# Performance work log

Hardware: AMD Instinct MI355X
Metric: run time of the kernel (lower is better)

Reference implementation:

```python
import jax, jax.numpy as jnp
import numpy as np

B, S, P = 64, 1024, 1024
D_IN, D, OUT = 50, 300, 1024
LN_EPS = 1e-6  # custom LayerNorm in repo-style code (a_2/b_2, eps=1e-6)


def setup_inputs() -> dict:
    key = jax.random.key(0)
    ks = jax.random.split(key, 16)
    std = 1e-4  # matches torch .normal_(mean=0, std=0.0001)
    return {
        "x": jax.random.normal(ks[0], (B, S, D_IN), jnp.float32),
        "matrix_embed": jax.random.normal(ks[1], (D_IN, D), jnp.float32),
        "past": jax.random.normal(ks[2], (B, P, D_IN), jnp.float32),
        "w_pt": jax.random.normal(ks[3], (D_IN, D), jnp.float32) * std,
        "b_pt": jax.random.normal(ks[4], (1, D), jnp.float32) * std,
        "w_pg": jax.random.normal(ks[5], (D_IN, D), jnp.float32) * std,
        "b_pg": jax.random.normal(ks[6], (1, D), jnp.float32) * std,
        "w_ps": jax.random.normal(ks[7], (D_IN, D), jnp.float32) * std,
        "b_ps": jax.random.normal(ks[8], (1, D), jnp.float32) * std,
        "w_ex": jax.random.normal(ks[9], (D_IN, D), jnp.float32) * std,
        "b_ex": jax.random.normal(ks[10], (1, D), jnp.float32) * std,
        "ln_g": jnp.ones((D,), jnp.float32),
        "ln_b": jnp.zeros((D,), jnp.float32),
        "W1": jax.random.normal(ks[11], (D, D), jnp.float32) * 0.05,
        "b1": jnp.zeros((D,), jnp.float32),
        "W2": jax.random.normal(ks[12], (D, OUT), jnp.float32) * 0.05,
        "b2": jnp.zeros((OUT,), jnp.float32),
    }


def _layernorm(h, g, b):
    mu = jnp.mean(h, axis=-1, keepdims=True)
    var = jnp.mean(jnp.square(h - mu), axis=-1, keepdims=True)
    return g * (h - mu) / jnp.sqrt(var + LN_EPS) + b


def reference(x, matrix_embed, past, w_pt, b_pt, w_pg, b_pg, w_ps, b_ps,
              w_ex, b_ex, ln_g, ln_b, W1, b1, W2, b2):
    # token: [B,S,300]
    token = _layernorm(x @ matrix_embed, ln_g, ln_b)
    past_token = jnp.tanh(x @ w_pt + b_pt)          # [B,S,300]
    past_vector = jnp.tanh(past @ w_pg + b_pg)      # [B,P,300]
    past_gate = jax.nn.sigmoid(jnp.einsum('bsd,bpd->bsp', past_token, past_vector))
    past_state = jnp.tanh(past @ w_ps + b_ps)       # [B,P,300]
    pre_state = past_gate @ past_state              # [B,S,300]
    expose_vector = jnp.tanh(x @ w_ex + b_ex)       # [B,S,300]
    expose_gate = jax.nn.sigmoid(jnp.einsum('bsd,btd->bst', expose_vector, pre_state))
    filter_token = token + expose_gate @ pre_state  # [B,S,300]
    # output MLP (dropout is identity in eval mode)
    h = jax.nn.relu(filter_token @ W1 + b1)
    return h @ W2 + b2
```

## Files before the change

kernel.cpp:

```cpp
#include <hip/hip_runtime.h>
#include <hip/hip_bf16.h>
#include <math.h>

typedef __attribute__((ext_vector_type(8))) short bf16x8;
typedef __attribute__((ext_vector_type(4))) float f32x4;

__device__ inline float bf2f(short u) {
  union { float f; unsigned int i; } v;
  v.i = ((unsigned int)(unsigned short)u) << 16;
  return v.f;
}
__device__ inline short f2bf(float f) {
  union { float f; unsigned int i; } v; v.f = f;
  unsigned int r = v.i + 0x7fff + ((v.i >> 16) & 1);
  return (short)(r >> 16);
}

__global__ void pad_rows(const float* __restrict__ src, short* __restrict__ dst,
                         int C, int Cp, int total) {
  int i = blockIdx.x * 256 + threadIdx.x;
  if (i >= total) return;
  int r = i / Cp, c = i - r * Cp;
  dst[i] = f2bf(c < C ? src[(size_t)r * C + c] : 0.f);
}

__global__ void pad_T(const float* __restrict__ src, short* __restrict__ dst,
                      int K, int N, int Kp, int total) {
  int i = blockIdx.x * 256 + threadIdx.x;
  if (i >= total) return;
  int n = i / Kp, k = i - n * Kp;
  dst[i] = f2bf((k < K && n < N) ? src[(size_t)k * N + n] : 0.f);
}

__global__ __launch_bounds__(256) void transpose_pd(const short* __restrict__ in,
                                                    short* __restrict__ out) {
  __shared__ unsigned int T[64][32];
  const int b = blockIdx.z, p0 = blockIdx.x * 64, d0 = blockIdx.y * 64;
  const short* ib = in + (size_t)b * 1024 * 320;
  short* ob = out + (size_t)b * 320 * 1024;
  for (int i = threadIdx.x; i < 512; i += 256) {
    int p = i >> 3, g = i & 7;
    uint4 v = *(const uint4*)&ib[(size_t)(p0 + p) * 320 + d0 + g * 8];
    int s = p & 31;
    T[p][(4 * g + 0) ^ s] = v.x;
    T[p][(4 * g + 1) ^ s] = v.y;
    T[p][(4 * g + 2) ^ s] = v.z;
    T[p][(4 * g + 3) ^ s] = v.w;
  }
  __syncthreads();
  for (int i = threadIdx.x; i < 512; i += 256) {
    int d = i >> 3, g = i & 7;
    int w0 = d >> 1;
    __align__(16) unsigned short tmp[8];
#pragma unroll
    for (int j = 0; j < 8; ++j) {
      int p = g * 8 + j;
      unsigned int val = T[p][w0 ^ (p & 31)];
      tmp[j] = (d & 1) ? (unsigned short)(val >> 16) : (unsigned short)(val & 0xffff);
    }
    *(uint4*)&ob[(size_t)(d0 + d) * 1024 + p0 + g * 8] = *(const uint4*)tmp;
  }
}

template<int NT, int MODE>
__global__ __launch_bounds__(512) void gemm_ep(
    const short* __restrict__ A, const short* __restrict__ Bt, int K,
    const float* __restrict__ bias, int biasN,
    void* __restrict__ outp, int outStride)
{
  __shared__ __align__(16) short Bst[NT][40];
  const int tid = threadIdx.x;
  const int wave = tid >> 6, lane = tid & 63;
  const int m = lane & 15, quad = lane >> 4;
  const int row0 = blockIdx.x * 128 + wave * 16;
  const int n0 = blockIdx.y * NT;

  f32x4 zero = {0.f, 0.f, 0.f, 0.f};
  f32x4 acc[NT / 16];
#pragma unroll
  for (int i = 0; i < NT / 16; ++i) acc[i] = zero;

  const short* arow = A + (size_t)(row0 + m) * K;

  for (int k0 = 0; k0 < K; k0 += 32) {
    __syncthreads();
    for (int idx = tid; idx < NT * 4; idx += 512) {
      int n = idx >> 2, kc = (idx & 3) << 3;
      *(uint4*)&Bst[n][kc] = *(const uint4*)&Bt[(size_t)(n0 + n) * K + k0 + kc];
    }
    __syncthreads();
    bf16x8 af = *(const bf16x8*)(arow + k0 + quad * 8);
#pragma unroll
    for (int nt = 0; nt < NT / 16; ++nt) {
      bf16x8 bf = *(const bf16x8*)&Bst[nt * 16 + m][quad * 8];
      acc[nt] = __builtin_amdgcn_mfma_f32_16x16x32_bf16(af, bf, acc[nt], 0, 0, 0);
    }
  }

#pragma unroll
  for (int nt = 0; nt < NT / 16; ++nt) {
#pragma unroll
    for (int r = 0; r < 4; ++r) {
      int row = row0 + quad * 4 + r;
      int col = n0 + nt * 16 + m;
      float v = acc[nt][r];
      if (MODE != 0) v += (col < biasN) ? bias[col] : 0.f;
      if (MODE == 1) v = tanhf(v);
      if (MODE == 2) v = fmaxf(v, 0.f);
      if (MODE == 3)
        ((float*)outp)[(size_t)row * outStride + col] = v;
      else
        ((short*)outp)[(size_t)row * outStride + col] = f2bf(v);
    }
  }
}

__global__ __launch_bounds__(256) void ln_rows(short* __restrict__ tp,
                                               const float* __restrict__ g,
                                               const float* __restrict__ bb) {
  const int wave = threadIdx.x >> 6, lane = threadIdx.x & 63;
  const int row = blockIdx.x * 4 + wave;
  short* p = tp + (size_t)row * 320;
  float vals[5], s = 0.f, ss = 0.f;
#pragma unroll
  for (int i = 0; i < 5; ++i) {
    int c = lane + i * 64;
    float v = (c < 300) ? bf2f(p[c]) : 0.f;
    vals[i] = v; s += v; ss += v * v;
  }
#pragma unroll
  for (int off = 32; off > 0; off >>= 1) { s += __shfl_down(s, off); ss += __shfl_down(ss, off); }
  s = __shfl(s, 0); ss = __shfl(ss, 0);
  const float mu = s * (1.f / 300.f);
  const float rstd = rsqrtf(ss * (1.f / 300.f) - mu * mu + 1e-6f);
#pragma unroll
  for (int i = 0; i < 5; ++i) {
    int c = lane + i * 64;
    float v = (c < 300) ? (g[c] * (vals[i] - mu) * rstd + bb[c]) : 0.f;
    p[c] = f2bf(v);
  }
}

__device__ inline void gload16(const short* g, short* l) {
  __builtin_amdgcn_global_load_lds((const __attribute__((address_space(1))) void*)g,
                                   (__attribute__((address_space(3))) void*)l, 16, 0, 0);
}
__device__ inline void block_sync() {
  asm volatile("s_waitcnt vmcnt(0) lgkmcnt(0)" ::: "memory");
  __builtin_amdgcn_s_barrier();
  __builtin_amdgcn_sched_barrier(0);
}

__global__ __launch_bounds__(512, 2) void attn_v6(
    const short* __restrict__ Qm, const short* __restrict__ Km,
    const short* __restrict__ VT, const short* __restrict__ tokp,
    short* __restrict__ Outp)
{
  __shared__ __align__(16) short KsL[2][10240];
  __shared__ __align__(16) short VsL[2][10240];

  const int tid = threadIdx.x;
  const int wave = tid >> 6, lane = tid & 63;
  const int m = lane & 15, quad = lane >> 4;
  const int b = blockIdx.x;
  const int qrow0 = b * 1024 + blockIdx.y * 128;
  const size_t kbase = (size_t)b * 1024 * 320;
  const short* vtb = VT + (size_t)b * 320 * 1024;

  const short* src[5];
  int dst[5];
#pragma unroll
  for (int j = 0; j < 5; ++j) {
    int c = j * 512 + tid;
    if (c < 1280) {
      int p = c / 40, ch = c - p * 40;
      src[j] = Km + kbase + (size_t)p * 320 + ((ch ^ (p & 7)) << 3);
      dst[j] = c << 3;
    } else {
      int cv = c - 1280;
      int d = cv >> 2, ch = cv & 3;
      src[j] = vtb + (size_t)d * 1024 + ((ch ^ (d & 3)) << 3);
      dst[j] = cv << 3;
    }
  }
  const bool j2K = (wave < 4);

  auto stage = [&](int pt) {
    const int bb = pt & 1;
    gload16(src[0] + (size_t)pt * 10240, &KsL[bb][dst[0]]);
    gload16(src[1] + (size_t)pt * 10240, &KsL[bb][dst[1]]);
    if (j2K) gload16(src[2] + (size_t)pt * 10240, &KsL[bb][dst[2]]);
    else     gload16(src[2] + (size_t)pt * 32,    &VsL[bb][dst[2]]);
    gload16(src[3] + (size_t)pt * 32, &VsL[bb][dst[3]]);
    gload16(src[4] + (size_t)pt * 32, &VsL[bb][dst[4]]);
  };

  bf16x8 qf[10];
  const short* qb = Qm + (size_t)(qrow0 + wave * 16 + m) * 320;
#pragma unroll
  for (int c = 0; c < 10; ++c)
    qf[c] = *(const bf16x8*)(qb + c * 32 + quad * 8);

  f32x4 zero = {0.f, 0.f, 0.f, 0.f};
  f32x4 o[20];
#pragma unroll
  for (int i = 0; i < 20; ++i) o[i] = zero;

  const int vch = (quad ^ (m & 3)) << 3;
  const unsigned oddq = (unsigned)(quad & 1);

  stage(0);
  block_sync();

  for (int pt = 0; pt < 32; ++pt) {
    if (pt < 31) stage(pt + 1);
    const short* Kc = &KsL[pt & 1][0];
    const short* Vc = &VsL[pt & 1][0];

    f32x4 sl = zero, sh = zero;
#pragma unroll
    for (int c = 0; c < 10; ++c) {
      int ch0 = ((4 * c + quad) ^ (m & 7)) << 3;
      bf16x8 k0 = *(const bf16x8*)&Kc[m * 320 + ch0];
      bf16x8 k1 = *(const bf16x8*)&Kc[(m + 16) * 320 + ch0];
      sl = __builtin_amdgcn_mfma_f32_16x16x32_bf16(k0, qf[c], sl, 0, 0, 0);
      sh = __builtin_amdgcn_mfma_f32_16x16x32_bf16(k1, qf[c], sh, 0, 0, 0);
    }

    float e0[4], e1[4];
#pragma unroll
    for (int r = 0; r < 4; ++r) {
      e0[r] = 1.f / (1.f + __expf(-sl[r]));
      e1[r] = 1.f / (1.f + __expf(-sh[r]));
    }
    int w0, w1, w2, w3;
    asm("v_cvt_pk_bf16_f32 %0, %1, %2" : "=v"(w0) : "v"(e0[0]), "v"(e0[1]));
    asm("v_cvt_pk_bf16_f32 %0, %1, %2" : "=v"(w1) : "v"(e0[2]), "v"(e0[3]));
    asm("v_cvt_pk_bf16_f32 %0, %1, %2" : "=v"(w2) : "v"(e1[0]), "v"(e1[1]));
    asm("v_cvt_pk_bf16_f32 %0, %1, %2" : "=v"(w3) : "v"(e1[2]), "v"(e1[3]));

    int x0 = w0, y0 = w2, x1 = w1, y1 = w3;
    asm volatile("v_permlane32_swap_b32 %0, %1" : "+v"(x0), "+v"(y0));
    asm volatile("v_permlane32_swap_b32 %0, %1" : "+v"(x1), "+v"(y1));
    int sx0 = __builtin_amdgcn_ds_swizzle(x0, 0x401f);
    int sy0 = __builtin_amdgcn_ds_swizzle(y0, 0x401f);
    int sx1 = __builtin_amdgcn_ds_swizzle(x1, 0x401f);
    int sy1 = __builtin_amdgcn_ds_swizzle(y1, 0x401f);
    union { int i[4]; bf16x8 v; } pu;
    pu.i[0] = oddq ? sy0 : x0;
    pu.i[1] = oddq ? sy1 : x1;
    pu.i[2] = oddq ? y0 : sx0;
    pu.i[3] = oddq ? y1 : sx1;
    bf16x8 pa = pu.v;

#pragma unroll
    for (int dt = 0; dt < 20; ++dt) {
      bf16x8 vb = *(const bf16x8*)&Vc[(dt * 16 + m) * 32 + vch];
      o[dt] = __builtin_amdgcn_mfma_f32_16x16x32_bf16(pa, vb, o[dt], 0, 0, 0);
    }

    block_sync();
  }

#pragma unroll
  for (int dt = 0; dt < 20; ++dt)
#pragma unroll
    for (int r = 0; r < 4; ++r) {
      const size_t row = (size_t)qrow0 + wave * 16 + quad * 4 + r;
      const int col = dt * 16 + m;
      float val = o[dt][r];
      if (tokp) val += bf2f(tokp[row * 320 + col]);
      Outp[row * 320 + col] = f2bf(val);
    }
}

extern "C" void kernel_launch(void* const* d_in, const int* in_sizes, int n_in,
                              void* d_out, int out_size, void* d_ws, size_t ws_size,
                              hipStream_t stream)
{
  const float* x    = (const float*)d_in[0];
  const float* me   = (const float*)d_in[1];
  const float* past = (const float*)d_in[2];
  const float* wpt  = (const float*)d_in[3];
  const float* bpt  = (const float*)d_in[4];
  const float* wpg  = (const float*)d_in[5];
  const float* bpg  = (const float*)d_in[6];
  const float* wps  = (const float*)d_in[7];
  const float* bps  = (const float*)d_in[8];
  const float* wex  = (const float*)d_in[9];
  const float* bex  = (const float*)d_in[10];
  const float* lng  = (const float*)d_in[11];
  const float* lnb  = (const float*)d_in[12];
  const float* W1   = (const float*)d_in[13];
  const float* b1   = (const float*)d_in[14];
  const float* W2   = (const float*)d_in[15];
  const float* b2   = (const float*)d_in[16];
  float* out = (float*)d_out;

  char* ws = (char*)d_ws;
  size_t off = 0;
  auto alloc = [&](size_t bytes) -> char* {
    char* p = ws + off; off += (bytes + 255) & ~(size_t)255; return p;
  };
  const size_t RB = 65536ull;
  short* xp    = (short*)alloc(RB * 64 * 2);
  short* pastp = (short*)alloc(RB * 64 * 2);
  short* wmeT  = (short*)alloc(320 * 64 * 2);
  short* wptT  = (short*)alloc(320 * 64 * 2);
  short* wpgT  = (short*)alloc(320 * 64 * 2);
  short* wpsT  = (short*)alloc(320 * 64 * 2);
  short* wexT  = (short*)alloc(320 * 64 * 2);
  short* w1T   = (short*)alloc(320 * 320 * 2);
  short* w2T   = (short*)alloc(1024ull * 320 * 2);
  short* buf0  = (short*)alloc(RB * 320 * 2);
  short* buf1  = (short*)alloc(RB * 320 * 2);
  short* buf2  = (short*)alloc(RB * 320 * 2);
  short* buf3  = (short*)alloc(RB * 320 * 2);
  short* vtbuf = (short*)alloc(RB * 320 * 2);

  {
    int total = 65536 * 64;
    pad_rows<<<dim3((total + 255) / 256), 256, 0, stream>>>(x, xp, 50, 64, total);
    pad_rows<<<dim3((total + 255) / 256), 256, 0, stream>>>(past, pastp, 50, 64, total);
  }
  {
    int t = 320 * 64;
    dim3 g((t + 255) / 256);
    pad_T<<<g, 256, 0, stream>>>(me,  wmeT, 50, 300, 64, t);
    pad_T<<<g, 256, 0, stream>>>(wpt, wptT, 50, 300, 64, t);
    pad_T<<<g, 256, 0, stream>>>(wpg, wpgT, 50, 300, 64, t);
    pad_T<<<g, 256, 0, stream>>>(wps, wpsT, 50, 300, 64, t);
    pad_T<<<g, 256, 0, stream>>>(wex, wexT, 50, 300, 64, t);
  }
  { int t = 320 * 320;  pad_T<<<(t + 255) / 256, 256, 0, stream>>>(W1, w1T, 300, 300, 320, t); }
  { int t = 1024 * 320; pad_T<<<(t + 255) / 256, 256, 0, stream>>>(W2, w2T, 300, 1024, 320, t); }

  dim3 g512(512, 1);
  dim3 tgrid(16, 5, 64);
  gemm_ep<320, 1><<<g512, 512, 0, stream>>>(xp,    wptT, 64, bpt, 300, buf0, 320);
  gemm_ep<320, 1><<<g512, 512, 0, stream>>>(pastp, wpgT, 64, bpg, 300, buf1, 320);
  gemm_ep<320, 1><<<g512, 512, 0, stream>>>(pastp, wpsT, 64, bps, 300, buf2, 320);
  transpose_pd<<<tgrid, 256, 0, stream>>>(buf2, vtbuf);

  attn_v6<<<dim3(64, 8), 512, 0, stream>>>(buf0, buf1, vtbuf, nullptr, buf3);

  gemm_ep<320, 0><<<g512, 512, 0, stream>>>(xp, wmeT, 64, nullptr, 0, buf1, 320);
  ln_rows<<<16384, 256, 0, stream>>>(buf1, lng, lnb);
  gemm_ep<320, 1><<<g512, 512, 0, stream>>>(xp, wexT, 64, bex, 300, buf2, 320);

  transpose_pd<<<tgrid, 256, 0, stream>>>(buf3, vtbuf);

  attn_v6<<<dim3(64, 8), 512, 0, stream>>>(buf2, buf3, vtbuf, buf1, buf0);

  gemm_ep<320, 2><<<g512, 512, 0, stream>>>(buf0, w1T, 320, b1, 300, buf3, 320);
  gemm_ep<256, 3><<<dim3(512, 4), 512, 0, stream>>>(buf3, w2T, 320, b2, 1024, out, 1024);
}
```

Measured before the change: 0.9999 ms.

## Fuse input padding, paired K=50 projections and LayerNorm into one small GEMM kernel

Adds a gemm_small kernel that reads the fp32 x/past rows directly, converts and pads them to bf16 in registers, and computes one or two 300-wide projections per launch with fused tanh or LayerNorm epilogues. This removes the two pad_rows passes, the separate LayerNorm pass and three gemm_ep launches, and it reuses one loaded A tile for two weight matrices. Buffers are remapped so the token output sits in buf2 for the second attention. The trade-offs are strided, unvectorised fp32 A loads (50-float rows), weight B fragments read straight from global memory without LDS staging, and high register use from 20 accumulators.

```diff
diff --git a/kernel.cpp b/kernel.cpp
--- a/kernel.cpp
+++ b/kernel.cpp
@@ -14,14 +14,6 @@
   union { float f; unsigned int i; } v; v.f = f;
   unsigned int r = v.i + 0x7fff + ((v.i >> 16) & 1);
   return (short)(r >> 16);
-}
-
-__global__ void pad_rows(const float* __restrict__ src, short* __restrict__ dst,
-                         int C, int Cp, int total) {
-  int i = blockIdx.x * 256 + threadIdx.x;
-  if (i >= total) return;
-  int r = i / Cp, c = i - r * Cp;
-  dst[i] = f2bf(c < C ? src[(size_t)r * C + c] : 0.f);
 }
 
 __global__ void pad_T(const float* __restrict__ src, short* __restrict__ dst,
@@ -115,29 +107,85 @@
   }
 }
 
-__global__ __launch_bounds__(256) void ln_rows(short* __restrict__ tp,
-                                               const float* __restrict__ g,
-                                               const float* __restrict__ bb) {
-  const int wave = threadIdx.x >> 6, lane = threadIdx.x & 63;
-  const int row = blockIdx.x * 4 + wave;
-  short* p = tp + (size_t)row * 320;
-  float vals[5], s = 0.f, ss = 0.f;
-#pragma unroll
-  for (int i = 0; i < 5; ++i) {
-    int c = lane + i * 64;
-    float v = (c < 300) ? bf2f(p[c]) : 0.f;
-    vals[i] = v; s += v; ss += v * v;
-  }
-#pragma unroll
-  for (int off = 32; off > 0; off >>= 1) { s += __shfl_down(s, off); ss += __shfl_down(ss, off); }
-  s = __shfl(s, 0); ss = __shfl(ss, 0);
-  const float mu = s * (1.f / 300.f);
-  const float rstd = rsqrtf(ss * (1.f / 300.f) - mu * mu + 1e-6f);
-#pragma unroll
-  for (int i = 0; i < 5; ++i) {
-    int c = lane + i * 64;
-    float v = (c < 300) ? (g[c] * (vals[i] - mu) * rstd + bb[c]) : 0.f;
-    p[c] = f2bf(v);
+template<int NOUT, int M0, int M1>
+__global__ __launch_bounds__(512) void gemm_small(
+    const float* __restrict__ A,
+    const short* __restrict__ B0, const float* __restrict__ p00, const float* __restrict__ p01,
+    const short* __restrict__ B1, const float* __restrict__ p10, const float* __restrict__ p11,
+    short* __restrict__ out0, short* __restrict__ out1)
+{
+  const int tid = threadIdx.x;
+  const int wave = tid >> 6, lane = tid & 63;
+  const int m = lane & 15, quad = lane >> 4;
+  const int row = blockIdx.x * 128 + wave * 16 + m;
+
+  bf16x8 af[2];
+#pragma unroll
+  for (int c = 0; c < 2; ++c) {
+    union { short s[8]; bf16x8 v; } u;
+#pragma unroll
+    for (int j = 0; j < 8; ++j) {
+      int k = c * 32 + quad * 8 + j;
+      u.s[j] = f2bf(k < 50 ? A[(size_t)row * 50 + k] : 0.f);
+    }
+    af[c] = u.v;
+  }
+
+#pragma unroll
+  for (int o = 0; o < NOUT; ++o) {
+    const short* Bt = o ? B1 : B0;
+    const float* pa = o ? p10 : p00;
+    const float* pb = o ? p11 : p01;
+    short* outp = o ? out1 : out0;
+    const int mode = o ? M1 : M0;
+
+    f32x4 acc[20];
+#pragma unroll
+    for (int i = 0; i < 20; ++i) acc[i] = {0.f, 0.f, 0.f, 0.f};
+#pragma unroll
+    for (int c = 0; c < 2; ++c) {
+      bf16x8 bf[20];
+#pragma unroll
+      for (int nt = 0; nt < 20; ++nt)
+        bf[nt] = *(const bf16x8*)&Bt[(size_t)(nt * 16 + m) * 64 + c * 32 + quad * 8];
+#pragma unroll
+      for (int nt = 0; nt < 20; ++nt)
+        acc[nt] = __builtin_amdgcn_mfma_f32_16x16x32_bf16(af[c], bf[nt], acc[nt], 0, 0, 0);
+    }
+
+    const int rbase = blockIdx.x * 128 + wave * 16 + quad * 4;
+    if (mode == 1) {
+#pragma unroll
+      for (int r = 0; r < 4; ++r) {
+        const size_t rw = (size_t)(rbase + r) * 320;
+#pragma unroll
+        for (int nt = 0; nt < 20; ++nt) {
+          int col = nt * 16 + m;
+          float v = acc[nt][r] + ((col < 300) ? pa[col] : 0.f);
+          outp[rw + col] = f2bf(tanhf(v));
+        }
+      }
+    } else {
+#pragma unroll
+      for (int r = 0; r < 4; ++r) {
+        float s = 0.f, ss = 0.f;
+#pragma unroll
+        for (int nt = 0; nt < 20; ++nt) { float v = acc[nt][r]; s += v; ss += v * v; }
+#pragma unroll
+        for (int off = 8; off > 0; off >>= 1) {
+          s += __shfl_xor(s, off); ss += __shfl_xor(ss, off);
+        }
+        const float mu = s * (1.f / 300.f);
+        const float rstd = rsqrtf(ss * (1.f / 300.f) - mu * mu + 1e-6f);
+        const size_t rw = (size_t)(rbase + r) * 320;
+#pragma unroll
+        for (int nt = 0; nt < 20; ++nt) {
+          int col = nt * 16 + m;
+          float v = (col < 300) ? (pa[col] * (acc[nt][r] - mu) * rstd + pb[col]) : 0.f;
+          outp[rw + col] = f2bf(v);
+        }
+      }
+    }
   }
 }
 
@@ -303,8 +351,6 @@
     char* p = ws + off; off += (bytes + 255) & ~(size_t)255; return p;
   };
   const size_t RB = 65536ull;
-  short* xp    = (short*)alloc(RB * 64 * 2);
-  short* pastp = (short*)alloc(RB * 64 * 2);
   short* wmeT  = (short*)alloc(320 * 64 * 2);
   short* wptT  = (short*)alloc(320 * 64 * 2);
   short* wpgT  = (short*)alloc(320 * 64 * 2);
@@ -319,11 +365,6 @@
   short* vtbuf = (short*)alloc(RB * 320 * 2);
 
   {
-    int total = 65536 * 64;
-    pad_rows<<<dim3((total + 255) / 256), 256, 0, stream>>>(x, xp, 50, 64, total);
-    pad_rows<<<dim3((total + 255) / 256), 256, 0, stream>>>(past, pastp, 50, 64, total);
-  }
-  {
     int t = 320 * 64;
     dim3 g((t + 255) / 256);
     pad_T<<<g, 256, 0, stream>>>(me,  wmeT, 50, 300, 64, t);
@@ -335,23 +376,19 @@
   { int t = 320 * 320;  pad_T<<<(t + 255) / 256, 256, 0, stream>>>(W1, w1T, 300, 300, 320, t); }
   { int t = 1024 * 320; pad_T<<<(t + 255) / 256, 256, 0, stream>>>(W2, w2T, 300, 1024, 320, t); }
 
-  dim3 g512(512, 1);
   dim3 tgrid(16, 5, 64);
-  gemm_ep<320, 1><<<g512, 512, 0, stream>>>(xp,    wptT, 64, bpt, 300, buf0, 320);
-  gemm_ep<320, 1><<<g512, 512, 0, stream>>>(pastp, wpgT, 64, bpg, 300, buf1, 320);
-  gemm_ep<320, 1><<<g512, 512, 0, stream>>>(pastp, wpsT, 64, bps, 300, buf2, 320);
+
+  gemm_small<2, 1, 1><<<512, 512, 0, stream>>>(past, wpgT, bpg, nullptr,
+                                               wpsT, bps, nullptr, buf1, buf2);
   transpose_pd<<<tgrid, 256, 0, stream>>>(buf2, vtbuf);
-
+  gemm_small<2, 1, 4><<<512, 512, 0, stream>>>(x, wptT, bpt, nullptr,
+                                               wmeT, lng, lnb, buf0, buf2);
   attn_v6<<<dim3(64, 8), 512, 0, stream>>>(buf0, buf1, vtbuf, nullptr, buf3);
-
-  gemm_ep<320, 0><<<g512, 512, 0, stream>>>(xp, wmeT, 64, nullptr, 0, buf1, 320);
-  ln_rows<<<16384, 256, 0, stream>>>(buf1, lng, lnb);
-  gemm_ep<320, 1><<<g512, 512, 0, stream>>>(xp, wexT, 64, bex, 300, buf2, 320);
-
+  gemm_small<1, 1, 1><<<512, 512, 0, stream>>>(x, wexT, bex, nullptr,
+                                               nullptr, nullptr, nullptr, buf1, nullptr);
   transpose_pd<<<tgrid, 256, 0, stream>>>(buf3, vtbuf);
-
-  attn_v6<<<dim3(64, 8), 512, 0, stream>>>(buf2, buf3, vtbuf, buf1, buf0);
-
-  gemm_ep<320, 2><<<g512, 512, 0, stream>>>(buf0, w1T, 320, b1, 300, buf3, 320);
+  attn_v6<<<dim3(64, 8), 512, 0, stream>>>(buf1, buf3, vtbuf, buf2, buf0);
+
+  gemm_ep<320, 2><<<dim3(512, 1), 512, 0, stream>>>(buf0, w1T, 320, b1, 300, buf3, 320);
   gemm_ep<256, 3><<<dim3(512, 4), 512, 0, stream>>>(buf3, w2T, 320, b2, 1024, out, 1024);
 }
```

Result: slower. 1.039 ms (+3.9%).

## Add double-buffered LDS-staged GEMM with 256-row tiles for output MLP

Applied to the files above, without the earlier changes.

Adds a new GEMM kernel that stages the weight tile into LDS with async global-to-LDS loads, double-buffered across K steps and XOR-swizzled. Each wave computes two 16-row MFMA tiles, so every block covers 256 rows instead of 128. The two output MLP GEMMs (W1 and W2) now use it, aiming at more reuse of the B tile and less redundant weight traffic. The cost is higher register pressure from doubled accumulators, a barrier on every K step, and half as many blocks.

```diff
diff --git a/kernel.cpp b/kernel.cpp
--- a/kernel.cpp
+++ b/kernel.cpp
@@ -115,6 +115,98 @@
   }
 }
 
+__device__ inline void gload16(const short* g, short* l) {
+  __builtin_amdgcn_global_load_lds((const __attribute__((address_space(1))) void*)g,
+                                   (__attribute__((address_space(3))) void*)l, 16, 0, 0);
+}
+__device__ inline void block_sync() {
+  asm volatile("s_waitcnt vmcnt(0) lgkmcnt(0)" ::: "memory");
+  __builtin_amdgcn_s_barrier();
+  __builtin_amdgcn_sched_barrier(0);
+}
+
+template<int NT, int MODE>
+__global__ __launch_bounds__(512) void gemm_big(
+    const short* __restrict__ A, const short* __restrict__ Bt, int K,
+    const float* __restrict__ bias, int biasN,
+    void* __restrict__ outp, int outStride)
+{
+  constexpr int NTT = NT / 16;
+  constexpr int JCNT = (NT * 4 + 511) / 512;
+  __shared__ __align__(16) short Bst[2][NT * 32];
+
+  const int tid = threadIdx.x;
+  const int wave = tid >> 6, lane = tid & 63;
+  const int m = lane & 15, quad = lane >> 4;
+  const int row0 = blockIdx.x * 256 + wave * 32;
+  const int n0 = blockIdx.y * NT;
+
+  const short* sp[JCNT];
+  int sd[JCNT];
+#pragma unroll
+  for (int j = 0; j < JCNT; ++j) {
+    int c = j * 512 + tid;
+    if (c < NT * 4) {
+      int n = c >> 2, ch = c & 3;
+      sp[j] = Bt + (size_t)(n0 + n) * K + ((ch ^ ((n >> 2) & 3)) << 3);
+      sd[j] = c << 3;
+    }
+  }
+  auto stage = [&](int it) {
+#pragma unroll
+    for (int j = 0; j < JCNT; ++j) {
+      int c = j * 512 + tid;
+      if (c < NT * 4) gload16(sp[j] + it * 32, &Bst[it & 1][sd[j]]);
+    }
+  };
+
+  f32x4 zero = {0.f, 0.f, 0.f, 0.f};
+  f32x4 acc[2][NTT];
+#pragma unroll
+  for (int h = 0; h < 2; ++h)
+#pragma unroll
+    for (int i = 0; i < NTT; ++i) acc[h][i] = zero;
+
+  const short* ar0 = A + (size_t)(row0 + m) * K;
+  const short* ar1 = A + (size_t)(row0 + 16 + m) * K;
+  const int rch = (quad ^ ((m >> 2) & 3)) << 3;
+
+  stage(0);
+  block_sync();
+
+  const int KIT = K >> 5;
+  for (int it = 0; it < KIT; ++it) {
+    bf16x8 a0 = *(const bf16x8*)(ar0 + it * 32 + quad * 8);
+    bf16x8 a1 = *(const bf16x8*)(ar1 + it * 32 + quad * 8);
+    if (it + 1 < KIT) stage(it + 1);
+    const short* Bc = &Bst[it & 1][0];
+#pragma unroll
+    for (int nt = 0; nt < NTT; ++nt) {
+      bf16x8 bf = *(const bf16x8*)&Bc[(nt * 16 + m) * 32 + rch];
+      acc[0][nt] = __builtin_amdgcn_mfma_f32_16x16x32_bf16(a0, bf, acc[0][nt], 0, 0, 0);
+      acc[1][nt] = __builtin_amdgcn_mfma_f32_16x16x32_bf16(a1, bf, acc[1][nt], 0, 0, 0);
+    }
+    block_sync();
+  }
+
+#pragma unroll
+  for (int h = 0; h < 2; ++h)
+#pragma unroll
+    for (int nt = 0; nt < NTT; ++nt)
+#pragma unroll
+      for (int r = 0; r < 4; ++r) {
+        int row = row0 + h * 16 + quad * 4 + r;
+        int col = n0 + nt * 16 + m;
+        float v = acc[h][nt][r];
+        v += (col < biasN) ? bias[col] : 0.f;
+        if (MODE == 2) v = fmaxf(v, 0.f);
+        if (MODE == 3)
+          ((float*)outp)[(size_t)row * outStride + col] = v;
+        else
+          ((short*)outp)[(size_t)row * outStride + col] = f2bf(v);
+      }
+}
+
 __global__ __launch_bounds__(256) void ln_rows(short* __restrict__ tp,
                                                const float* __restrict__ g,
                                                const float* __restrict__ bb) {
@@ -139,16 +231,6 @@
     float v = (c < 300) ? (g[c] * (vals[i] - mu) * rstd + bb[c]) : 0.f;
     p[c] = f2bf(v);
   }
-}
-
-__device__ inline void gload16(const short* g, short* l) {
-  __builtin_amdgcn_global_load_lds((const __attribute__((address_space(1))) void*)g,
-                                   (__attribute__((address_space(3))) void*)l, 16, 0, 0);
-}
-__device__ inline void block_sync() {
-  asm volatile("s_waitcnt vmcnt(0) lgkmcnt(0)" ::: "memory");
-  __builtin_amdgcn_s_barrier();
-  __builtin_amdgcn_sched_barrier(0);
 }
 
 __global__ __launch_bounds__(512, 2) void attn_v6(
@@ -352,6 +434,6 @@
 
   attn_v6<<<dim3(64, 8), 512, 0, stream>>>(buf2, buf3, vtbuf, buf1, buf0);
 
-  gemm_ep<320, 2><<<g512, 512, 0, stream>>>(buf0, w1T, 320, b1, 300, buf3, 320);
-  gemm_ep<256, 3><<<dim3(512, 4), 512, 0, stream>>>(buf3, w2T, 320, b2, 1024, out, 1024);
-}
+  gemm_big<320, 2><<<dim3(256, 1), 512, 0, stream>>>(buf0, w1T, 320, b1, 300, buf3, 320);
+  gemm_big<256, 3><<<dim3(256, 4), 512, 0, stream>>>(buf3, w2T, 320, b2, 1024, out, 1024);
+}
```

Measured after the change: 983.6 us. About the same (-1.6%).
